# Kernel tuning notes

Hardware: AMD Instinct MI355X
Metric: run time of the kernel (lower is better)

Reference implementation:

```python
import jax, jax.numpy as jnp
import numpy as np

N = 50000
NEG_SLOPE = 0.2


def add_self_loops(edge_index, n):
    loop = jnp.arange(n, dtype=edge_index.dtype)
    return jnp.concatenate([edge_index, jnp.stack([loop, loop])], axis=1)


def gatv2_conv(x, edge_index, Wl, bl, Wr, br, att, bias):
    """PyG GATv2Conv (share_weights=False, concat=True, add_self_loops applied by caller).
    x: [N, Fin]; edge_index: [2, E] with row0=src(j), row1=dst(i); att: [H, D].
    Returns (out [N, H*D], alpha [E, H])."""
    src, dst = edge_index[0], edge_index[1]
    H, D = att.shape
    n = x.shape[0]
    xl = (x @ Wl + bl).reshape(n, H, D)   # source-side transform
    xr = (x @ Wr + br).reshape(n, H, D)   # target-side transform
    e = jax.nn.leaky_relu(xl[src] + xr[dst], NEG_SLOPE)        # [E, H, D]
    logit = jnp.einsum('ehd,hd->eh', e, att)                    # [E, H]
    # segment softmax over edges grouped by target node
    lmax = jax.ops.segment_max(logit, dst, num_segments=n)      # [N, H]
    ex = jnp.exp(logit - lmax[dst])
    denom = jax.ops.segment_sum(ex, dst, num_segments=n)
    alpha = ex / denom[dst]                                     # [E, H]
    out = jax.ops.segment_sum(alpha[:, :, None] * xl[src], dst, num_segments=n)  # [N, H, D]
    return out.reshape(n, H * D) + bias, alpha


def setup_inputs() -> dict:
    key = jax.random.key(0)
    ks = jax.random.split(key, 16)
    E = 400000
    x = jax.random.normal(ks[0], (N, 23), dtype=jnp.float32)
    edge_index = jax.random.randint(ks[1], (2, E), 0, N, dtype=jnp.int64)
    H1, D1 = 8, 64
    F1 = H1 * D1  # 512
    s = 0.1
    return {
        'x': x,
        'edge_index': edge_index,
        'Wl1': jax.random.normal(ks[2], (23, F1), dtype=jnp.float32) * s,
        'bl1': jnp.zeros((F1,), jnp.float32),
        'Wr1': jax.random.normal(ks[3], (23, F1), dtype=jnp.float32) * s,
        'br1': jnp.zeros((F1,), jnp.float32),
        'att1': jax.random.normal(ks[4], (H1, D1), dtype=jnp.float32) * s,
        'bias1': jnp.zeros((F1,), jnp.float32),
        'Wl2': jax.random.normal(ks[5], (F1, 1), dtype=jnp.float32) * s,
        'bl2': jnp.zeros((1,), jnp.float32),
        'Wr2': jax.random.normal(ks[6], (F1, 1), dtype=jnp.float32) * s,
        'br2': jnp.zeros((1,), jnp.float32),
        'att2': jax.random.normal(ks[7], (1, 1), dtype=jnp.float32) * s,
        'bias2': jnp.zeros((1,), jnp.float32),
    }


def reference(x, edge_index, Wl1, bl1, Wr1, br1, att1, bias1,
              Wl2, bl2, Wr2, br2, att2, bias2):
    ei = add_self_loops(edge_index, N)
    h, _ = gatv2_conv(x, ei, Wl1, bl1, Wr1, br1, att1, bias1)
    h = jax.nn.relu(h)
    h, alpha = gatv2_conv(h, ei, Wl2, bl2, Wr2, br2, att2, bias2)
    return h, alpha
```

## Files before the change

kernel.cpp:

```cpp
#include <hip/hip_runtime.h>
#include <math.h>

#define NN 50000
#define E0 400000
#define EE 450000
#define FF 512
#define G1 2048
#define NPB ((NN + G1 - 1) / G1)
#define EPB ((EE + G1 - 1) / G1)
#define WAVES_TOTAL (G1 * 4)
#define SCANB 49
#define LOG2E 1.44269504f

typedef _Float16 h2 __attribute__((ext_vector_type(2)));

__device__ __forceinline__ h2 uas_h2(unsigned u) { union { unsigned u; h2 h; } c; c.u = u; return c.h; }
__device__ __forceinline__ unsigned h2as_u(h2 h) { union { unsigned u; h2 h; } c; c.h = h; return c.u; }
__device__ __forceinline__ float leaky(float v) { return fmaxf(v, 0.2f * v); }

__global__ __launch_bounds__(256) void k_predeg(
    const float* __restrict__ x,
    const float* __restrict__ Wl1, const float* __restrict__ bl1,
    const float* __restrict__ Wr1, const float* __restrict__ br1,
    const int* __restrict__ ei,
    unsigned* __restrict__ xlh, unsigned* __restrict__ xrh, int* __restrict__ deg)
{
    __shared__ float sx[NPB * 23];
    int b = blockIdx.x, t = threadIdx.x;
    int i0 = b * NPB;
    int i1 = i0 + NPB; if (i1 > NN) i1 = NN;
    int nf = (i1 - i0) * 23;

    {
        int e = b * EPB + t;
        if (t < EPB && e < EE) {
            int dst = (e < E0) ? ei[E0 + e] : (e - E0);
            atomicAdd(&deg[dst], 1);
        }
    }

    for (int k = t; k < nf; k += 256) sx[k] = x[i0 * 23 + k];

    int c0 = 2 * t, c1 = 2 * t + 1;
    float wl0[23], wl1v[23], wr0[23], wr1v[23];
#pragma unroll
    for (int r = 0; r < 23; r++) {
        wl0[r]  = Wl1[r * FF + c0];
        wl1v[r] = Wl1[r * FF + c1];
        wr0[r]  = Wr1[r * FF + c0];
        wr1v[r] = Wr1[r * FF + c1];
    }
    float bl0 = bl1[c0], bl1s = bl1[c1];
    float br0 = br1[c0], br1s = br1[c1];
    __syncthreads();

    for (int n = 0; n < i1 - i0; n++) {
        float a0 = bl0, a1 = bl1s, b0v = br0, b1v = br1s;
#pragma unroll
        for (int r = 0; r < 23; r++) {
            float xv = sx[n * 23 + r];
            a0  += xv * wl0[r];
            a1  += xv * wl1v[r];
            b0v += xv * wr0[r];
            b1v += xv * wr1v[r];
        }
        h2 hl = { (_Float16)a0,  (_Float16)a1  };
        h2 hr = { (_Float16)b0v, (_Float16)b1v };
        xlh[(size_t)(i0 + n) * 256 + t] = h2as_u(hl);
        xrh[(size_t)(i0 + n) * 256 + t] = h2as_u(hr);
    }
}

__global__ __launch_bounds__(256) void k_scan(
    const int* __restrict__ deg, unsigned* __restrict__ flag,
    int* __restrict__ offs, int* __restrict__ cur)
{
    __shared__ int wsum[4];
    __shared__ int s_prev;
    int b = blockIdx.x, t = threadIdx.x;
    int base = b * 1024 + t * 4;
    int v0 = (base     < NN) ? deg[base]     : 0;
    int v1 = (base + 1 < NN) ? deg[base + 1] : 0;
    int v2 = (base + 2 < NN) ? deg[base + 2] : 0;
    int v3 = (base + 3 < NN) ? deg[base + 3] : 0;
    int tsum = v0 + v1 + v2 + v3;
    int lane = t & 63, wv = t >> 6;
    int sc = tsum;
#pragma unroll
    for (int o = 1; o < 64; o <<= 1) {
        int u = __shfl_up(sc, o, 64);
        if (lane >= o) sc += u;
    }
    if (lane == 63) wsum[wv] = sc;
    __syncthreads();
    int woff = 0;
    for (int k = 0; k < wv; k++) woff += wsum[k];
    int btot = wsum[0] + wsum[1] + wsum[2] + wsum[3];

    if (t == 0) atomicExch(&flag[b], (unsigned)btot + 1u);
    int contrib = 0;
    if (t < b) {
        unsigned f;
        do { f = atomicAdd(&flag[t], 0u); } while (f == 0u);
        contrib = (int)(f - 1u);
    }
    if (t < 64) {
#pragma unroll
        for (int o = 32; o > 0; o >>= 1) contrib += __shfl_xor(contrib, o, 64);
        if (t == 0) s_prev = contrib;
    }
    __syncthreads();
    int add = s_prev;
    int ex = add + woff + sc - tsum;
    if (base     < NN) { offs[base]     = ex;                cur[base]     = ex; }
    if (base + 1 < NN) { offs[base + 1] = ex + v0;           cur[base + 1] = ex + v0; }
    if (base + 2 < NN) { offs[base + 2] = ex + v0 + v1;      cur[base + 2] = ex + v0 + v1; }
    if (base + 3 < NN) { offs[base + 3] = ex + v0 + v1 + v2; cur[base + 3] = ex + v0 + v1 + v2; }
    if (b == SCANB - 1 && t == 255) offs[NN] = add + btot;
}

__global__ void k_scatter(const int* __restrict__ ei, int* __restrict__ cur,
                          int* __restrict__ src_s, int* __restrict__ eid_s)
{
    int e = blockIdx.x * blockDim.x + threadIdx.x;
    if (e >= EE) return;
    int src, dst;
    if (e < E0) { src = ei[e]; dst = ei[E0 + e]; }
    else        { src = e - E0; dst = src; }
    int p = atomicAdd(&cur[dst], 1);
    src_s[p] = src;
    eid_s[p] = e;
}

__global__ __launch_bounds__(256) void k_layer1(
    const uint4* __restrict__ xlh, const uint4* __restrict__ xrh,
    const float* __restrict__ att, const float* __restrict__ bias1,
    const float* __restrict__ Wl2, const float* __restrict__ bl2,
    const float* __restrict__ Wr2, const float* __restrict__ br2,
    const int* __restrict__ offs, const int* __restrict__ src_s,
    float* __restrict__ xl2, float* __restrict__ xr2)
{
    int t = threadIdx.x;
    int l = t & 63;
    int wid = blockIdx.x * 4 + (t >> 6);

    float4 atA = ((const float4*)att)[2 * l];
    float4 atB = ((const float4*)att)[2 * l + 1];
    h2 a6_0 = { (_Float16)(0.6f * LOG2E * atA.x), (_Float16)(0.6f * LOG2E * atA.y) };
    h2 a6_1 = { (_Float16)(0.6f * LOG2E * atA.z), (_Float16)(0.6f * LOG2E * atA.w) };
    h2 a6_2 = { (_Float16)(0.6f * LOG2E * atB.x), (_Float16)(0.6f * LOG2E * atB.y) };
    h2 a6_3 = { (_Float16)(0.6f * LOG2E * atB.z), (_Float16)(0.6f * LOG2E * atB.w) };
    h2 a4_0 = { (_Float16)(0.4f * LOG2E * atA.x), (_Float16)(0.4f * LOG2E * atA.y) };
    h2 a4_1 = { (_Float16)(0.4f * LOG2E * atA.z), (_Float16)(0.4f * LOG2E * atA.w) };
    h2 a4_2 = { (_Float16)(0.4f * LOG2E * atB.x), (_Float16)(0.4f * LOG2E * atB.y) };
    h2 a4_3 = { (_Float16)(0.4f * LOG2E * atB.z), (_Float16)(0.4f * LOG2E * atB.w) };
    float bl2v = bl2[0], br2v = br2[0];

    for (int i = wid; i < NN; i += WAVES_TOTAL) {
        uint4 xq = xrh[(size_t)i * 64 + l];
        h2 q0 = uas_h2(xq.x), q1 = uas_h2(xq.y), q2 = uas_h2(xq.z), q3 = uas_h2(xq.w);

        float s = 0.f;
        h2 A0 = { 0, 0 }, A1 = { 0, 0 }, A2 = { 0, 0 }, A3 = { 0, 0 };

        int beg = offs[i], deg = offs[i + 1] - beg;

        for (int cb = 0; cb < deg; cb += 64) {
            int cnt = deg - cb; if (cnt > 64) cnt = 64;
            int myj = (l < cnt) ? src_s[beg + cb + l] : 0;

            int j0 = __builtin_amdgcn_readlane(myj, 0);
            uint4 r0 = xlh[(size_t)j0 * 64 + l];
            uint4 r1 = r0;
            if (cnt > 1) r1 = xlh[(size_t)__builtin_amdgcn_readlane(myj, 1) * 64 + l];

            for (int p = 0; p < cnt; p++) {
                uint4 rn = r0;
                if (p + 2 < cnt)
                    rn = xlh[(size_t)__builtin_amdgcn_readlane(myj, p + 2) * 64 + l];

                h2 p0 = uas_h2(r0.x), p1 = uas_h2(r0.y), p2 = uas_h2(r0.z), p3 = uas_h2(r0.w);
                h2 t0 = p0 + q0, t1 = p1 + q1, t2 = p2 + q2, t3 = p3 + q3;
                h2 b0 = uas_h2(h2as_u(t0) & 0x7fff7fffu);
                h2 b1 = uas_h2(h2as_u(t1) & 0x7fff7fffu);
                h2 b2 = uas_h2(h2as_u(t2) & 0x7fff7fffu);
                h2 b3 = uas_h2(h2as_u(t3) & 0x7fff7fffu);
                float part = 0.f;
                part = __builtin_amdgcn_fdot2(a6_0, t0, part, false);
                part = __builtin_amdgcn_fdot2(a4_0, b0, part, false);
                part = __builtin_amdgcn_fdot2(a6_1, t1, part, false);
                part = __builtin_amdgcn_fdot2(a4_1, b1, part, false);
                part = __builtin_amdgcn_fdot2(a6_2, t2, part, false);
                part = __builtin_amdgcn_fdot2(a4_2, b2, part, false);
                part = __builtin_amdgcn_fdot2(a6_3, t3, part, false);
                part = __builtin_amdgcn_fdot2(a4_3, b3, part, false);
                part += __shfl_xor(part, 1, 64);
                part += __shfl_xor(part, 2, 64);
                part += __shfl_xor(part, 4, 64);
                float w = exp2f(part);
                s += w;
                _Float16 wh = (_Float16)w;
                h2 w2 = { wh, wh };
                A0 += w2 * p0;
                A1 += w2 * p1;
                A2 += w2 * p2;
                A3 += w2 * p3;
                r0 = r1; r1 = rn;
            }
        }

        float inv = 1.f / s;
        float4 bA = ((const float4*)bias1)[2 * l];
        float4 bB = ((const float4*)bias1)[2 * l + 1];
        float h0 = fmaxf(fmaf((float)A0[0], inv, bA.x), 0.f);
        float h1 = fmaxf(fmaf((float)A0[1], inv, bA.y), 0.f);
        float h2v = fmaxf(fmaf((float)A1[0], inv, bA.z), 0.f);
        float h3 = fmaxf(fmaf((float)A1[1], inv, bA.w), 0.f);
        float h4 = fmaxf(fmaf((float)A2[0], inv, bB.x), 0.f);
        float h5 = fmaxf(fmaf((float)A2[1], inv, bB.y), 0.f);
        float h6 = fmaxf(fmaf((float)A3[0], inv, bB.z), 0.f);
        float h7 = fmaxf(fmaf((float)A3[1], inv, bB.w), 0.f);

        float4 wlA = ((const float4*)Wl2)[2 * l];
        float4 wlB = ((const float4*)Wl2)[2 * l + 1];
        float4 wrA = ((const float4*)Wr2)[2 * l];
        float4 wrB = ((const float4*)Wr2)[2 * l + 1];
        float pl = h0 * wlA.x + h1 * wlA.y + h2v * wlA.z + h3 * wlA.w
                 + h4 * wlB.x + h5 * wlB.y + h6 * wlB.z + h7 * wlB.w;
        float pr = h0 * wrA.x + h1 * wrA.y + h2v * wrA.z + h3 * wrA.w
                 + h4 * wrB.x + h5 * wrB.y + h6 * wrB.z + h7 * wrB.w;
#pragma unroll
        for (int o = 32; o > 0; o >>= 1) {
            pl += __shfl_xor(pl, o, 64);
            pr += __shfl_xor(pr, o, 64);
        }
        if (l == 0) {
            xl2[i] = pl + bl2v;
            xr2[i] = pr + br2v;
        }
    }
}

__global__ void k_layer2(const float* __restrict__ xl2, const float* __restrict__ xr2,
                         const float* __restrict__ att2, const float* __restrict__ bias2,
                         const int* __restrict__ offs, const int* __restrict__ src_s,
                         const int* __restrict__ eid_s, float* __restrict__ out)
{
    int i = blockIdx.x * blockDim.x + threadIdx.x;
    if (i >= NN) return;
    int beg = offs[i], end = offs[i + 1];
    float xri = xr2[i];
    float a2l = att2[0] * LOG2E;
    float s = 0.f, num = 0.f;
    for (int p = beg; p < end; p++) {
        float v = xl2[src_s[p]];
        float w = exp2f(leaky(v + xri) * a2l);
        s += w;
        num = fmaf(w, v, num);
    }
    out[i] = num / s + bias2[0];
    float inv = 1.f / s;
    for (int p = beg; p < end; p++) {
        float v = xl2[src_s[p]];
        float w = exp2f(leaky(v + xri) * a2l);
        out[NN + eid_s[p]] = w * inv;
    }
}

extern "C" void kernel_launch(void* const* d_in, const int* in_sizes, int n_in,
                              void* d_out, int out_size, void* d_ws, size_t ws_size,
                              hipStream_t stream)
{
    const float* x     = (const float*)d_in[0];
    const int*   ei    = (const int*)d_in[1];
    const float* Wl1   = (const float*)d_in[2];
    const float* bl1   = (const float*)d_in[3];
    const float* Wr1   = (const float*)d_in[4];
    const float* br1   = (const float*)d_in[5];
    const float* att1  = (const float*)d_in[6];
    const float* bias1 = (const float*)d_in[7];
    const float* Wl2   = (const float*)d_in[8];
    const float* bl2   = (const float*)d_in[9];
    const float* Wr2   = (const float*)d_in[10];
    const float* br2   = (const float*)d_in[11];
    const float* att2  = (const float*)d_in[12];
    const float* bias2 = (const float*)d_in[13];
    float* out = (float*)d_out;

    char* ws = (char*)d_ws;
    unsigned* xlh = (unsigned*)ws; ws += (size_t)NN * 256 * 4;
    unsigned* xrh = (unsigned*)ws; ws += (size_t)NN * 256 * 4;
    float* xl2  = (float*)ws;      ws += (size_t)NN * 4;
    float* xr2  = (float*)ws;      ws += (size_t)NN * 4;
    int* deg    = (int*)ws;        ws += (size_t)NN * 4;
    unsigned* flag = (unsigned*)ws; ws += (size_t)64 * 4;
    int* offs   = (int*)ws;        ws += (size_t)(NN + 1) * 4;
    int* cur    = (int*)ws;        ws += (size_t)NN * 4;
    int* src_s  = (int*)ws;        ws += (size_t)EE * 4;
    int* eid_s  = (int*)ws;        ws += (size_t)EE * 4;

    hipMemsetAsync(deg, 0, (size_t)(NN + 64) * 4, stream);

    k_predeg<<<G1, 256, 0, stream>>>(x, Wl1, bl1, Wr1, br1, ei, xlh, xrh, deg);
    k_scan<<<SCANB, 256, 0, stream>>>(deg, flag, offs, cur);
    k_scatter<<<(EE + 255) / 256, 256, 0, stream>>>(ei, cur, src_s, eid_s);
    k_layer1<<<G1, 256, 0, stream>>>((const uint4*)xlh, (const uint4*)xrh,
                                     att1, bias1, Wl2, bl2, Wr2, br2,
                                     offs, src_s, xl2, xr2);
    k_layer2<<<(NN + 255) / 256, 256, 0, stream>>>(xl2, xr2, att2, bias2,
                                                   offs, src_s, eid_s, out);
}
```

Baseline: 252.4 us.

## Compute layer-1 projections with MFMA and pack src/eid into one array

The first-layer node projection (x @ Wl1, x @ Wr1) moves from scalar FMA loops to 16x16x32 f16 MFMA instructions. Each wave handles one half of one weight matrix, and blocks process 5 tiles of 16 nodes. The grid drops to 625 blocks with a reworked degree-count split. Separately, the sorted source and edge-id arrays are merged into one uint2 array, so layer2 fetches both with a single load. This adds f16 rounding of the inputs and weights, and the 2-byte strided output stores may coalesce poorly.

```diff
diff --git a/kernel.cpp b/kernel.cpp
--- a/kernel.cpp
+++ b/kernel.cpp
@@ -6,13 +6,16 @@
 #define EE 450000
 #define FF 512
 #define G1 2048
-#define NPB ((NN + G1 - 1) / G1)
-#define EPB ((EE + G1 - 1) / G1)
 #define WAVES_TOTAL (G1 * 4)
 #define SCANB 49
 #define LOG2E 1.44269504f
+#define PREB 625
+#define PRES 5
+#define PEPB (EE / PREB)
 
 typedef _Float16 h2 __attribute__((ext_vector_type(2)));
+typedef _Float16 f16x8 __attribute__((ext_vector_type(8)));
+typedef float f32x4 __attribute__((ext_vector_type(4)));
 
 __device__ __forceinline__ h2 uas_h2(unsigned u) { union { unsigned u; h2 h; } c; c.u = u; return c.h; }
 __device__ __forceinline__ unsigned h2as_u(h2 h) { union { unsigned u; h2 h; } c; c.h = h; return c.u; }
@@ -23,51 +26,62 @@
     const float* __restrict__ Wl1, const float* __restrict__ bl1,
     const float* __restrict__ Wr1, const float* __restrict__ br1,
     const int* __restrict__ ei,
-    unsigned* __restrict__ xlh, unsigned* __restrict__ xrh, int* __restrict__ deg)
-{
-    __shared__ float sx[NPB * 23];
+    _Float16* __restrict__ xlh, _Float16* __restrict__ xrh, int* __restrict__ deg)
+{
     int b = blockIdx.x, t = threadIdx.x;
-    int i0 = b * NPB;
-    int i1 = i0 + NPB; if (i1 > NN) i1 = NN;
-    int nf = (i1 - i0) * 23;
-
-    {
-        int e = b * EPB + t;
-        if (t < EPB && e < EE) {
-            int dst = (e < E0) ? ei[E0 + e] : (e - E0);
-            atomicAdd(&deg[dst], 1);
-        }
-    }
-
-    for (int k = t; k < nf; k += 256) sx[k] = x[i0 * 23 + k];
-
-    int c0 = 2 * t, c1 = 2 * t + 1;
-    float wl0[23], wl1v[23], wr0[23], wr1v[23];
-#pragma unroll
-    for (int r = 0; r < 23; r++) {
-        wl0[r]  = Wl1[r * FF + c0];
-        wl1v[r] = Wl1[r * FF + c1];
-        wr0[r]  = Wr1[r * FF + c0];
-        wr1v[r] = Wr1[r * FF + c1];
-    }
-    float bl0 = bl1[c0], bl1s = bl1[c1];
-    float br0 = br1[c0], br1s = br1[c1];
-    __syncthreads();
-
-    for (int n = 0; n < i1 - i0; n++) {
-        float a0 = bl0, a1 = bl1s, b0v = br0, b1v = br1s;
-#pragma unroll
-        for (int r = 0; r < 23; r++) {
-            float xv = sx[n * 23 + r];
-            a0  += xv * wl0[r];
-            a1  += xv * wl1v[r];
-            b0v += xv * wr0[r];
-            b1v += xv * wr1v[r];
-        }
-        h2 hl = { (_Float16)a0,  (_Float16)a1  };
-        h2 hr = { (_Float16)b0v, (_Float16)b1v };
-        xlh[(size_t)(i0 + n) * 256 + t] = h2as_u(hl);
-        xrh[(size_t)(i0 + n) * 256 + t] = h2as_u(hr);
+    int w = t >> 6, l = t & 63;
+    int q = l >> 4;
+    int ln = l & 15;
+
+    for (int e = b * PEPB + t; e < b * PEPB + PEPB; e += 256) {
+        int dst = (e < E0) ? ei[E0 + e] : (e - E0);
+        atomicAdd(&deg[dst], 1);
+    }
+
+    const float* W  = (w < 2) ? Wl1 : Wr1;
+    const float* bv = (w < 2) ? bl1 : br1;
+    _Float16* dst16 = (w < 2) ? xlh : xrh;
+    int col0 = 256 * (w & 1);
+
+    f16x8 bf[16];
+    float bias[16];
+#pragma unroll
+    for (int n = 0; n < 16; n++) {
+        int col = col0 + 16 * n + ln;
+        bias[n] = bv[col];
+#pragma unroll
+        for (int j = 0; j < 8; j++) {
+            int k = q * 8 + j;
+            bf[n][j] = (k < 23) ? (_Float16)W[k * FF + col] : (_Float16)0.f;
+        }
+    }
+
+    for (int sidx = 0; sidx < PRES; sidx++) {
+        int sb = (b * PRES + sidx) * 16;
+        const float* xrow = x + (size_t)(sb + ln) * 23;
+        f16x8 af;
+#pragma unroll
+        for (int j = 0; j < 8; j++) {
+            int k = q * 8 + j;
+            af[j] = (k < 23) ? (_Float16)xrow[k] : (_Float16)0.f;
+        }
+
+        f32x4 acc[16];
+#pragma unroll
+        for (int n = 0; n < 16; n++) {
+            acc[n] = (f32x4){ bias[n], bias[n], bias[n], bias[n] };
+            acc[n] = __builtin_amdgcn_mfma_f32_16x16x32_f16(af, bf[n], acc[n], 0, 0, 0);
+        }
+
+#pragma unroll
+        for (int n = 0; n < 16; n++) {
+            int col = col0 + 16 * n + ln;
+#pragma unroll
+            for (int r = 0; r < 4; r++) {
+                int node = sb + q * 4 + r;
+                dst16[(size_t)node * FF + col] = (_Float16)acc[n][r];
+            }
+        }
     }
 }
 
@@ -120,7 +134,7 @@
 }
 
 __global__ void k_scatter(const int* __restrict__ ei, int* __restrict__ cur,
-                          int* __restrict__ src_s, int* __restrict__ eid_s)
+                          uint2* __restrict__ se_s)
 {
     int e = blockIdx.x * blockDim.x + threadIdx.x;
     if (e >= EE) return;
@@ -128,8 +142,7 @@
     if (e < E0) { src = ei[e]; dst = ei[E0 + e]; }
     else        { src = e - E0; dst = src; }
     int p = atomicAdd(&cur[dst], 1);
-    src_s[p] = src;
-    eid_s[p] = e;
+    se_s[p] = make_uint2((unsigned)src, (unsigned)e);
 }
 
 __global__ __launch_bounds__(256) void k_layer1(
@@ -137,7 +150,7 @@
     const float* __restrict__ att, const float* __restrict__ bias1,
     const float* __restrict__ Wl2, const float* __restrict__ bl2,
     const float* __restrict__ Wr2, const float* __restrict__ br2,
-    const int* __restrict__ offs, const int* __restrict__ src_s,
+    const int* __restrict__ offs, const uint2* __restrict__ se_s,
     float* __restrict__ xl2, float* __restrict__ xr2)
 {
     int t = threadIdx.x;
@@ -167,7 +180,7 @@
 
         for (int cb = 0; cb < deg; cb += 64) {
             int cnt = deg - cb; if (cnt > 64) cnt = 64;
-            int myj = (l < cnt) ? src_s[beg + cb + l] : 0;
+            int myj = (l < cnt) ? (int)se_s[beg + cb + l].x : 0;
 
             int j0 = __builtin_amdgcn_readlane(myj, 0);
             uint4 r0 = xlh[(size_t)j0 * 64 + l];
@@ -197,9 +210,9 @@
                 part += __shfl_xor(part, 1, 64);
                 part += __shfl_xor(part, 2, 64);
                 part += __shfl_xor(part, 4, 64);
-                float w = exp2f(part);
-                s += w;
-                _Float16 wh = (_Float16)w;
+                float wv = exp2f(part);
+                s += wv;
+                _Float16 wh = (_Float16)wv;
                 h2 w2 = { wh, wh };
                 A0 += w2 * p0;
                 A1 += w2 * p1;
@@ -243,8 +256,8 @@
 
 __global__ void k_layer2(const float* __restrict__ xl2, const float* __restrict__ xr2,
                          const float* __restrict__ att2, const float* __restrict__ bias2,
-                         const int* __restrict__ offs, const int* __restrict__ src_s,
-                         const int* __restrict__ eid_s, float* __restrict__ out)
+                         const int* __restrict__ offs, const uint2* __restrict__ se_s,
+                         float* __restrict__ out)
 {
     int i = blockIdx.x * blockDim.x + threadIdx.x;
     if (i >= NN) return;
@@ -253,7 +266,7 @@
     float a2l = att2[0] * LOG2E;
     float s = 0.f, num = 0.f;
     for (int p = beg; p < end; p++) {
-        float v = xl2[src_s[p]];
+        float v = xl2[se_s[p].x];
         float w = exp2f(leaky(v + xri) * a2l);
         s += w;
         num = fmaf(w, v, num);
@@ -261,9 +274,10 @@
     out[i] = num / s + bias2[0];
     float inv = 1.f / s;
     for (int p = beg; p < end; p++) {
-        float v = xl2[src_s[p]];
+        uint2 se = se_s[p];
+        float v = xl2[se.x];
         float w = exp2f(leaky(v + xri) * a2l);
-        out[NN + eid_s[p]] = w * inv;
+        out[NN + se.y] = w * inv;
     }
 }
 
@@ -288,25 +302,24 @@
     float* out = (float*)d_out;
 
     char* ws = (char*)d_ws;
-    unsigned* xlh = (unsigned*)ws; ws += (size_t)NN * 256 * 4;
-    unsigned* xrh = (unsigned*)ws; ws += (size_t)NN * 256 * 4;
+    _Float16* xlh = (_Float16*)ws; ws += (size_t)NN * FF * 2;
+    _Float16* xrh = (_Float16*)ws; ws += (size_t)NN * FF * 2;
     float* xl2  = (float*)ws;      ws += (size_t)NN * 4;
     float* xr2  = (float*)ws;      ws += (size_t)NN * 4;
     int* deg    = (int*)ws;        ws += (size_t)NN * 4;
     unsigned* flag = (unsigned*)ws; ws += (size_t)64 * 4;
     int* offs   = (int*)ws;        ws += (size_t)(NN + 1) * 4;
     int* cur    = (int*)ws;        ws += (size_t)NN * 4;
-    int* src_s  = (int*)ws;        ws += (size_t)EE * 4;
-    int* eid_s  = (int*)ws;        ws += (size_t)EE * 4;
+    uint2* se_s = (uint2*)ws;      ws += (size_t)EE * 8;
 
     hipMemsetAsync(deg, 0, (size_t)(NN + 64) * 4, stream);
 
-    k_predeg<<<G1, 256, 0, stream>>>(x, Wl1, bl1, Wr1, br1, ei, xlh, xrh, deg);
+    k_predeg<<<PREB, 256, 0, stream>>>(x, Wl1, bl1, Wr1, br1, ei, xlh, xrh, deg);
     k_scan<<<SCANB, 256, 0, stream>>>(deg, flag, offs, cur);
-    k_scatter<<<(EE + 255) / 256, 256, 0, stream>>>(ei, cur, src_s, eid_s);
+    k_scatter<<<(EE + 255) / 256, 256, 0, stream>>>(ei, cur, se_s);
     k_layer1<<<G1, 256, 0, stream>>>((const uint4*)xlh, (const uint4*)xrh,
                                      att1, bias1, Wl2, bl2, Wr2, br2,
-                                     offs, src_s, xl2, xr2);
+                                     offs, se_s, xl2, xr2);
     k_layer2<<<(NN + 255) / 256, 256, 0, stream>>>(xl2, xr2, att2, bias2,
-                                                   offs, src_s, eid_s, out);
-}
+                                                   offs, se_s, out);
+}
```

New measurement: 308.3 us. 22.2% more time.
